# Optimization experiments

Hardware: AMD Instinct MI355X
Metric: run time of the kernel (lower is better)

## Reference

```python
import jax, jax.numpy as jnp
import numpy as np


def setup_inputs() -> dict:
    key = jax.random.key(0)
    k1, k2 = jax.random.split(key)
    B, d, h = 65536, 256, 1024  # na = d//4 = 64, G = B//na = 1024, h = 4*d
    x = jax.random.normal(k1, (B, d), dtype=jnp.float32)
    A = 0.1 * jax.random.normal(k2, (d, h), dtype=jnp.float32)
    return {"x": x, "A": A}


def reference(x, A):
    # x: [B, d], A: [d, h] with h = 4*d, na = d // 4, G = B // na
    B, d = x.shape
    na = d // 4
    G = B // na
    n2 = 2 * na

    # bmm with broadcast A + SiLU -> [B, h]; reshape [B, 16, na], sum -> [B]
    J = jax.nn.silu(x @ A)                      # [B, h]
    j12 = J.reshape(B, 16, na).sum(axis=(1, 2)).reshape(G, na)  # [G, na]

    # kron(diag(j12), eye(2)) duplicates each diagonal entry onto a 2x2 identity
    diagvals = jnp.repeat(j12, 2, axis=1)        # [G, 2*na]

    # Final block matrix [[J11, J12], [J21, J22]] with J11=J22=0,
    # J12 = +diag, J21 = -diag, each expanded by kron with eye(2).
    idx = jnp.arange(n2)
    out = jnp.zeros((G, 4 * na, 4 * na), dtype=x.dtype)
    out = out.at[:, idx, n2 + idx].set(diagvals)    # top-right block diagonal
    out = out.at[:, n2 + idx, idx].set(-diagvals)   # bottom-left block diagonal
    return out
```

## Files before the change

### kernel.cpp

```cpp
#include <hip/hip_runtime.h>
#include <stdint.h>

typedef float    f32x4  __attribute__((ext_vector_type(4)));
typedef __bf16   bf16x8 __attribute__((ext_vector_type(8)));
typedef uint32_t u32x4  __attribute__((ext_vector_type(4)));
typedef unsigned short u16x4 __attribute__((ext_vector_type(4)));

#define AS1 __attribute__((address_space(1)))
#define AS3 __attribute__((address_space(3)))

__device__ __forceinline__ unsigned short f2bf_bits(float f) {
  uint32_t u = __builtin_bit_cast(uint32_t, f);
  u += 0x7fffu + ((u >> 16) & 1u);
  return (unsigned short)(u >> 16);
}

__global__ void k_transpose_cvt(const float* __restrict__ A,
                                unsigned short* __restrict__ At) {
  int n = blockIdx.x * blockDim.x + threadIdx.x;
  int o = n << 2;
  int col = o >> 8;
  int k   = o & 255;
  u16x4 v;
#pragma unroll
  for (int j = 0; j < 4; ++j) v[j] = f2bf_bits(A[(size_t)(k + j) * 1024 + col]);
  *reinterpret_cast<u16x4*>(At + o) = v;
}

__launch_bounds__(256, 4)
__global__ void k_gemm_fused(const float* __restrict__ x,
                             const unsigned short* __restrict__ At,
                             float* __restrict__ out) {
  __shared__ alignas(16) char lds[4][8192];

  const int tid  = threadIdx.x;
  const int lane = tid & 63;
  const int w    = tid >> 6;
  const int bIdx = blockIdx.x;
  const int brow = bIdx * 64;

  const int col = lane & 15;
  const int hi  = lane >> 4;

  uint32_t p0  = (uint32_t)(w * 2048 + lane * 16);
  uint32_t so0 = p0 ^ (((p0 >> 9) & 7u) << 4);
  uint32_t p1  = p0 + 1024u;
  uint32_t so1 = p1 ^ (((p1 >> 9) & 7u) << 4);

  {
    const char* t0 = (const char*)At;
    const char* t1 = (const char*)At + 8192;
    __builtin_amdgcn_global_load_lds((const AS1 uint32_t*)(t0 + so0),
                                     (AS3 uint32_t*)(lds[0] + w * 2048), 16, 0, 0);
    __builtin_amdgcn_global_load_lds((const AS1 uint32_t*)(t0 + so1),
                                     (AS3 uint32_t*)(lds[0] + w * 2048 + 1024), 16, 0, 0);
    __builtin_amdgcn_global_load_lds((const AS1 uint32_t*)(t1 + so0),
                                     (AS3 uint32_t*)(lds[1] + w * 2048), 16, 0, 0);
    __builtin_amdgcn_global_load_lds((const AS1 uint32_t*)(t1 + so1),
                                     (AS3 uint32_t*)(lds[1] + w * 2048 + 1024), 16, 0, 0);
  }
  __builtin_amdgcn_sched_barrier(0);

  bf16x8 xf[8];
  {
    const float* xr = x + (size_t)(brow + w * 16 + col) * 256;
#pragma unroll
    for (int s = 0; s < 8; ++s) {
      f32x4 a = __builtin_nontemporal_load(
          reinterpret_cast<const f32x4*>(xr + s * 32 + hi * 8));
      f32x4 b = __builtin_nontemporal_load(
          reinterpret_cast<const f32x4*>(xr + s * 32 + hi * 8 + 4));
      bf16x8 f;
      f[0] = (__bf16)a[0]; f[1] = (__bf16)a[1];
      f[2] = (__bf16)a[2]; f[3] = (__bf16)a[3];
      f[4] = (__bf16)b[0]; f[5] = (__bf16)b[1];
      f[6] = (__bf16)b[2]; f[7] = (__bf16)b[3];
      xf[s] = f;
    }
  }
  asm volatile("s_waitcnt vmcnt(0)" ::: "memory");

  uint32_t rbase = ((uint32_t)(col * 512 + hi * 16)) ^ ((uint32_t)(col & 7) << 4);

  float sums[4] = {0.f, 0.f, 0.f, 0.f};
  float* outblk = out + (size_t)bIdx * 65536;
  const f32x4 z4 = {0.f, 0.f, 0.f, 0.f};

  for (int tile = 0; tile < 64; ++tile) {
    {
      int pt = (tile + 2) & 63;
      const char* tsrc = (const char*)At + (size_t)pt * 8192;
      char* dst = lds[(tile + 2) & 3] + w * 2048;
      __builtin_amdgcn_global_load_lds((const AS1 uint32_t*)(tsrc + so0),
                                       (AS3 uint32_t*)dst, 16, 0, 0);
      __builtin_amdgcn_global_load_lds((const AS1 uint32_t*)(tsrc + so1),
                                       (AS3 uint32_t*)(dst + 1024), 16, 0, 0);
    }
    __builtin_amdgcn_sched_barrier(0);
    __builtin_nontemporal_store(
        z4, reinterpret_cast<f32x4*>(outblk + tile * 1024 + (tid << 2)));

    asm volatile("s_waitcnt vmcnt(7)\n\ts_barrier" ::: "memory");

    const char* buf = lds[tile & 3];
    bf16x8 bfr[8];
#pragma unroll
    for (int s = 0; s < 8; ++s) {
      uint32_t addr = rbase ^ ((uint32_t)s << 6);
      bfr[s] = __builtin_bit_cast(
          bf16x8, *reinterpret_cast<const u32x4*>(buf + addr));
    }
    f32x4 acc = {0.f, 0.f, 0.f, 0.f};
#pragma unroll
    for (int s = 0; s < 8; ++s)
      acc = __builtin_amdgcn_mfma_f32_16x16x32_bf16(xf[s], bfr[s], acc, 0, 0, 0);
#pragma unroll
    for (int j = 0; j < 4; ++j) {
      float z = acc[j];
      float sig = __builtin_amdgcn_rcpf(1.0f + __expf(-z));
      sums[j] += z * sig;
    }
  }

  asm volatile("s_waitcnt vmcnt(0)\n\ts_barrier" ::: "memory");

#pragma unroll
  for (int j = 0; j < 4; ++j) {
    float v = sums[j];
    v += __shfl_xor(v, 1, 64);
    v += __shfl_xor(v, 2, 64);
    v += __shfl_xor(v, 4, 64);
    v += __shfl_xor(v, 8, 64);
    sums[j] = v;
  }

  if (col == 0) {
#pragma unroll
    for (int j = 0; j < 4; ++j) {
      int c = w * 16 + hi * 4 + j;
      float s = sums[j];
      float* og = outblk;
      og[(2 * c) * 256 + 128 + 2 * c]     =  s;
      og[(2 * c + 1) * 256 + 129 + 2 * c] =  s;
      og[(128 + 2 * c) * 256 + 2 * c]     = -s;
      og[(129 + 2 * c) * 256 + 2 * c + 1] = -s;
    }
  }
}

extern "C" void kernel_launch(void* const* d_in, const int* in_sizes, int n_in,
                              void* d_out, int out_size, void* d_ws, size_t ws_size,
                              hipStream_t stream) {
  const float* x = (const float*)d_in[0];
  const float* A = (const float*)d_in[1];
  float* out = (float*)d_out;
  unsigned short* At = (unsigned short*)d_ws;

  k_transpose_cvt<<<256, 256, 0, stream>>>(A, At);
  k_gemm_fused<<<1024, 256, 0, stream>>>(x, At, out);
}
```

Before: 84.88 us.

## Split zero-fill and GEMM into separate blocks, write diagonals without overlap

```diff
diff --git a/kernel.cpp b/kernel.cpp
--- a/kernel.cpp
+++ b/kernel.cpp
@@ -28,16 +28,34 @@
 }
 
 __launch_bounds__(256, 4)
-__global__ void k_gemm_fused(const float* __restrict__ x,
-                             const unsigned short* __restrict__ At,
-                             float* __restrict__ out) {
+__global__ void k_main(const float* __restrict__ x,
+                       const unsigned short* __restrict__ At,
+                       float* __restrict__ out) {
   __shared__ alignas(16) char lds[4][8192];
 
-  const int tid  = threadIdx.x;
+  const int b   = blockIdx.x;
+  const int tid = threadIdx.x;
+  const int g   = b >> 1;
+  float* og = out + (size_t)g * 65536;
+
+  if (!(b & 1)) {
+    const int w = tid >> 6;
+    const int l = (tid >> 2) & 15;
+    const int q = tid & 3;
+    const f32x4 z4 = {0.f, 0.f, 0.f, 0.f};
+    for (int i = 0; i < 64; ++i) {
+      int r  = i * 4 + w;
+      int dl = ((r & 127) >> 4) + (r < 128 ? 8 : 0);
+      if (l != dl)
+        __builtin_nontemporal_store(
+            z4, reinterpret_cast<f32x4*>(og + r * 256 + l * 16 + q * 4));
+    }
+    return;
+  }
+
   const int lane = tid & 63;
   const int w    = tid >> 6;
-  const int bIdx = blockIdx.x;
-  const int brow = bIdx * 64;
+  const int brow = g * 64;
 
   const int col = lane & 15;
   const int hi  = lane >> 4;
@@ -68,13 +86,13 @@
     for (int s = 0; s < 8; ++s) {
       f32x4 a = __builtin_nontemporal_load(
           reinterpret_cast<const f32x4*>(xr + s * 32 + hi * 8));
-      f32x4 b = __builtin_nontemporal_load(
+      f32x4 bq = __builtin_nontemporal_load(
           reinterpret_cast<const f32x4*>(xr + s * 32 + hi * 8 + 4));
       bf16x8 f;
-      f[0] = (__bf16)a[0]; f[1] = (__bf16)a[1];
-      f[2] = (__bf16)a[2]; f[3] = (__bf16)a[3];
-      f[4] = (__bf16)b[0]; f[5] = (__bf16)b[1];
-      f[6] = (__bf16)b[2]; f[7] = (__bf16)b[3];
+      f[0] = (__bf16)a[0];  f[1] = (__bf16)a[1];
+      f[2] = (__bf16)a[2];  f[3] = (__bf16)a[3];
+      f[4] = (__bf16)bq[0]; f[5] = (__bf16)bq[1];
+      f[6] = (__bf16)bq[2]; f[7] = (__bf16)bq[3];
       xf[s] = f;
     }
   }
@@ -83,8 +101,6 @@
   uint32_t rbase = ((uint32_t)(col * 512 + hi * 16)) ^ ((uint32_t)(col & 7) << 4);
 
   float sums[4] = {0.f, 0.f, 0.f, 0.f};
-  float* outblk = out + (size_t)bIdx * 65536;
-  const f32x4 z4 = {0.f, 0.f, 0.f, 0.f};
 
   for (int tile = 0; tile < 64; ++tile) {
     {
@@ -96,11 +112,7 @@
       __builtin_amdgcn_global_load_lds((const AS1 uint32_t*)(tsrc + so1),
                                        (AS3 uint32_t*)(dst + 1024), 16, 0, 0);
     }
-    __builtin_amdgcn_sched_barrier(0);
-    __builtin_nontemporal_store(
-        z4, reinterpret_cast<f32x4*>(outblk + tile * 1024 + (tid << 2)));
-
-    asm volatile("s_waitcnt vmcnt(7)\n\ts_barrier" ::: "memory");
+    asm volatile("s_waitcnt vmcnt(4)\n\ts_barrier" ::: "memory");
 
     const char* buf = lds[tile & 3];
     bf16x8 bfr[8];
@@ -122,8 +134,6 @@
     }
   }
 
-  asm volatile("s_waitcnt vmcnt(0)\n\ts_barrier" ::: "memory");
-
 #pragma unroll
   for (int j = 0; j < 4; ++j) {
     float v = sums[j];
@@ -134,16 +144,31 @@
     sums[j] = v;
   }
 
+  float* sarr = reinterpret_cast<float*>(lds);
+  __syncthreads();
   if (col == 0) {
 #pragma unroll
-    for (int j = 0; j < 4; ++j) {
-      int c = w * 16 + hi * 4 + j;
-      float s = sums[j];
-      float* og = outblk;
-      og[(2 * c) * 256 + 128 + 2 * c]     =  s;
-      og[(2 * c + 1) * 256 + 129 + 2 * c] =  s;
-      og[(128 + 2 * c) * 256 + 2 * c]     = -s;
-      og[(129 + 2 * c) * 256 + 2 * c + 1] = -s;
+    for (int j = 0; j < 4; ++j) sarr[w * 16 + hi * 4 + j] = sums[j];
+  }
+  __syncthreads();
+  {
+    int r  = tid;
+    int c  = (r & 127) >> 1;
+    float s = sarr[c];
+    s = (r < 128) ? s : -s;
+    int dl = ((r & 127) >> 4) + (r < 128 ? 8 : 0);
+    int p  = r & 15;
+    float* lp = og + r * 256 + dl * 16;
+#pragma unroll
+    for (int q2 = 0; q2 < 4; ++q2) {
+      f32x4 v = {0.f, 0.f, 0.f, 0.f};
+      if ((p >> 2) == q2) {
+        v[0] = ((p & 3) == 0) ? s : 0.f;
+        v[1] = ((p & 3) == 1) ? s : 0.f;
+        v[2] = ((p & 3) == 2) ? s : 0.f;
+        v[3] = ((p & 3) == 3) ? s : 0.f;
+      }
+      __builtin_nontemporal_store(v, reinterpret_cast<f32x4*>(lp + q2 * 4));
     }
   }
 }
@@ -157,5 +182,5 @@
   unsigned short* At = (unsigned short*)d_ws;
 
   k_transpose_cvt<<<256, 256, 0, stream>>>(A, At);
-  k_gemm_fused<<<1024, 256, 0, stream>>>(x, At, out);
+  k_main<<<2048, 256, 0, stream>>>(x, At, out);
 }
```

Result: slower. 131.6 us (+55.0%).

## Split output zero-fill into separate diagonal fill kernel after GEMM sums

Applied to the files above, without the earlier changes.

```diff
diff --git a/kernel.cpp b/kernel.cpp
--- a/kernel.cpp
+++ b/kernel.cpp
@@ -28,16 +28,16 @@
 }
 
 __launch_bounds__(256, 4)
-__global__ void k_gemm_fused(const float* __restrict__ x,
-                             const unsigned short* __restrict__ At,
-                             float* __restrict__ out) {
+__global__ void k_gemm_sums(const float* __restrict__ x,
+                            const unsigned short* __restrict__ At,
+                            float* __restrict__ j12) {
   __shared__ alignas(16) char lds[4][8192];
 
   const int tid  = threadIdx.x;
   const int lane = tid & 63;
   const int w    = tid >> 6;
-  const int bIdx = blockIdx.x;
-  const int brow = bIdx * 64;
+  const int g    = blockIdx.x;
+  const int brow = g * 64;
 
   const int col = lane & 15;
   const int hi  = lane >> 4;
@@ -68,13 +68,13 @@
     for (int s = 0; s < 8; ++s) {
       f32x4 a = __builtin_nontemporal_load(
           reinterpret_cast<const f32x4*>(xr + s * 32 + hi * 8));
-      f32x4 b = __builtin_nontemporal_load(
+      f32x4 bq = __builtin_nontemporal_load(
           reinterpret_cast<const f32x4*>(xr + s * 32 + hi * 8 + 4));
       bf16x8 f;
-      f[0] = (__bf16)a[0]; f[1] = (__bf16)a[1];
-      f[2] = (__bf16)a[2]; f[3] = (__bf16)a[3];
-      f[4] = (__bf16)b[0]; f[5] = (__bf16)b[1];
-      f[6] = (__bf16)b[2]; f[7] = (__bf16)b[3];
+      f[0] = (__bf16)a[0];  f[1] = (__bf16)a[1];
+      f[2] = (__bf16)a[2];  f[3] = (__bf16)a[3];
+      f[4] = (__bf16)bq[0]; f[5] = (__bf16)bq[1];
+      f[6] = (__bf16)bq[2]; f[7] = (__bf16)bq[3];
       xf[s] = f;
     }
   }
@@ -83,8 +83,6 @@
   uint32_t rbase = ((uint32_t)(col * 512 + hi * 16)) ^ ((uint32_t)(col & 7) << 4);
 
   float sums[4] = {0.f, 0.f, 0.f, 0.f};
-  float* outblk = out + (size_t)bIdx * 65536;
-  const f32x4 z4 = {0.f, 0.f, 0.f, 0.f};
 
   for (int tile = 0; tile < 64; ++tile) {
     {
@@ -96,11 +94,7 @@
       __builtin_amdgcn_global_load_lds((const AS1 uint32_t*)(tsrc + so1),
                                        (AS3 uint32_t*)(dst + 1024), 16, 0, 0);
     }
-    __builtin_amdgcn_sched_barrier(0);
-    __builtin_nontemporal_store(
-        z4, reinterpret_cast<f32x4*>(outblk + tile * 1024 + (tid << 2)));
-
-    asm volatile("s_waitcnt vmcnt(7)\n\ts_barrier" ::: "memory");
+    asm volatile("s_waitcnt vmcnt(4)\n\ts_barrier" ::: "memory");
 
     const char* buf = lds[tile & 3];
     bf16x8 bfr[8];
@@ -110,19 +104,20 @@
       bfr[s] = __builtin_bit_cast(
           bf16x8, *reinterpret_cast<const u32x4*>(buf + addr));
     }
-    f32x4 acc = {0.f, 0.f, 0.f, 0.f};
+    f32x4 acc0 = {0.f, 0.f, 0.f, 0.f};
+    f32x4 acc1 = {0.f, 0.f, 0.f, 0.f};
 #pragma unroll
-    for (int s = 0; s < 8; ++s)
-      acc = __builtin_amdgcn_mfma_f32_16x16x32_bf16(xf[s], bfr[s], acc, 0, 0, 0);
+    for (int s = 0; s < 4; ++s) {
+      acc0 = __builtin_amdgcn_mfma_f32_16x16x32_bf16(xf[s],     bfr[s],     acc0, 0, 0, 0);
+      acc1 = __builtin_amdgcn_mfma_f32_16x16x32_bf16(xf[s + 4], bfr[s + 4], acc1, 0, 0, 0);
+    }
 #pragma unroll
     for (int j = 0; j < 4; ++j) {
-      float z = acc[j];
+      float z = acc0[j] + acc1[j];
       float sig = __builtin_amdgcn_rcpf(1.0f + __expf(-z));
       sums[j] += z * sig;
     }
   }
-
-  asm volatile("s_waitcnt vmcnt(0)\n\ts_barrier" ::: "memory");
 
 #pragma unroll
   for (int j = 0; j < 4; ++j) {
@@ -136,15 +131,37 @@
 
   if (col == 0) {
 #pragma unroll
-    for (int j = 0; j < 4; ++j) {
-      int c = w * 16 + hi * 4 + j;
-      float s = sums[j];
-      float* og = outblk;
-      og[(2 * c) * 256 + 128 + 2 * c]     =  s;
-      og[(2 * c + 1) * 256 + 129 + 2 * c] =  s;
-      og[(128 + 2 * c) * 256 + 2 * c]     = -s;
-      og[(129 + 2 * c) * 256 + 2 * c + 1] = -s;
+    for (int j = 0; j < 4; ++j)
+      j12[g * 64 + w * 16 + hi * 4 + j] = sums[j];
+  }
+}
+
+__launch_bounds__(256, 8)
+__global__ void k_fill_diag(const float* __restrict__ j12,
+                            float* __restrict__ out) {
+  const int tid = threadIdx.x;
+  const size_t base = (size_t)blockIdx.x * 32768;
+#pragma unroll 2
+  for (int i = 0; i < 32; ++i) {
+    size_t o = base + (size_t)i * 1024 + (tid << 2);
+    int gf = (int)(o & 65535);
+    int g  = (int)(o >> 16);
+    int rr = gf >> 8;
+    int cc = gf & 255;
+    int ii = rr & 127;
+    int dc = (rr < 128) ? (ii + 128) : ii;
+    float s = 0.f;
+    if ((dc >> 2) == (cc >> 2)) {
+      s = j12[g * 64 + (ii >> 1)];
+      if (rr >= 128) s = -s;
     }
+    int sl = dc & 3;
+    f32x4 v;
+    v[0] = (sl == 0) ? s : 0.f;
+    v[1] = (sl == 1) ? s : 0.f;
+    v[2] = (sl == 2) ? s : 0.f;
+    v[3] = (sl == 3) ? s : 0.f;
+    *reinterpret_cast<f32x4*>(out + o) = v;
   }
 }
 
@@ -155,7 +172,9 @@
   const float* A = (const float*)d_in[1];
   float* out = (float*)d_out;
   unsigned short* At = (unsigned short*)d_ws;
+  float* j12 = (float*)((char*)d_ws + 512 * 1024);
 
   k_transpose_cvt<<<256, 256, 0, stream>>>(A, At);
-  k_gemm_fused<<<1024, 256, 0, stream>>>(x, At, out);
+  k_gemm_sums<<<1024, 256, 0, stream>>>(x, At, j12);
+  k_fill_diag<<<2048, 256, 0, stream>>>(j12, out);
 }
```

After: 97.54 us. 14.9% more time.
